# Performance work log

Hardware: AMD Instinct MI355X
Metric: run time of the kernel (lower is better)

Reference implementation:

```python
import jax, jax.numpy as jnp
import numpy as np

HEADS = 4
DIM_HEAD = 32
DIM = 512
HIDDEN = HEADS * DIM_HEAD  # 128


def setup_inputs() -> dict:
    key = jax.random.key(0)
    k1, k2, k3, k4 = jax.random.split(key, 4)
    b, l = 8, 8192
    x = jax.random.normal(k1, (b, DIM, l), dtype=jnp.float32)
    # Conv1d kernel_size=1 weights stored as [out_ch, in_ch] (squeeze kernel dim)
    w_qkv = jax.random.normal(k2, (HIDDEN * 3, DIM), dtype=jnp.float32) * (1.0 / np.sqrt(DIM))
    w_out = jax.random.normal(k3, (DIM, HIDDEN), dtype=jnp.float32) * (1.0 / np.sqrt(HIDDEN))
    b_out = jax.random.normal(k4, (DIM,), dtype=jnp.float32) * 0.01
    return {"x": x, "w_qkv": w_qkv, "w_out": w_out, "b_out": b_out}


def reference(x, w_qkv, w_out, b_out):
    b, c, l = x.shape
    # 1x1 conv == channel matmul: [b, 3*hidden, l]
    qkv = jnp.einsum('oc,bcl->bol', w_qkv, x)
    # split into q, k, v each [b, heads, dim_head, l]
    qkv = qkv.reshape(b, 3, HEADS, DIM_HEAD, l)
    q, k, v = qkv[:, 0], qkv[:, 1], qkv[:, 2]
    k = jax.nn.softmax(k, axis=-1)  # softmax over sequence positions
    # context: [b, h, d, e] (small dim_head x dim_head per head)
    context = jnp.einsum('bhdn,bhen->bhde', k, v)
    out = jnp.einsum('bhde,bhdn->bhen', context, q)  # [b, h, e, l]
    out = out.reshape(b, HIDDEN, l)
    return jnp.einsum('oc,bcl->bol', w_out, out) + b_out[None, :, None]
```

## Files before the change

kernel.cpp:

```cpp
#include <hip/hip_runtime.h>
#include <math.h>
#include <stdint.h>


#define L_LEN 8192L
#define DIMC 512

typedef short bf16x8 __attribute__((ext_vector_type(8)));
typedef float f32x4 __attribute__((ext_vector_type(4)));

__device__ __forceinline__ unsigned short f2bf(float f) {
    uint32_t u = __float_as_uint(f);
    u += 0x7FFFu + ((u >> 16) & 1u);
    return (unsigned short)(u >> 16);
}
__device__ __forceinline__ void unpack8(uint4 u, float* f) {
    f[0] = __uint_as_float(u.x << 16); f[1] = __uint_as_float(u.x & 0xFFFF0000u);
    f[2] = __uint_as_float(u.y << 16); f[3] = __uint_as_float(u.y & 0xFFFF0000u);
    f[4] = __uint_as_float(u.z << 16); f[5] = __uint_as_float(u.z & 0xFFFF0000u);
    f[6] = __uint_as_float(u.w << 16); f[7] = __uint_as_float(u.w & 0xFFFF0000u);
}

#define GLOAD_LDS16(g, l) __builtin_amdgcn_global_load_lds( \
    (const __attribute__((address_space(1))) uint32_t*)(g), \
    (__attribute__((address_space(3))) uint32_t*)(l), 16, 0, 0)

__global__ __launch_bounds__(256)
void misc_kernel(const float* __restrict__ w, unsigned short* __restrict__ wb,
                 float* __restrict__ zbase)
{
    int idx = blockIdx.x * 256 + threadIdx.x;
    if (idx < 196608) wb[idx] = f2bf(w[idx]);
    else {
        int z = idx - 196608;
        if (z < 33792) zbase[z] = 0.0f;
    }
}

__global__ __launch_bounds__(256)
void xpose_cvt_kernel(const float* __restrict__ x, unsigned short* __restrict__ xb)
{
    const int b  = blockIdx.z;
    const int c0 = blockIdx.y * 64;
    const int l0 = blockIdx.x * 64;
    const float* xp = x + (long)b * DIMC * L_LEN;
    unsigned short* op = xb + (long)b * L_LEN * DIMC;
    __shared__ float tile[64][65];
    const int t = threadIdx.x;
    #pragma unroll
    for (int r = 0; r < 4; ++r) {
        int idx = t + 256 * r;
        int row = idx >> 4, col4 = (idx & 15) * 4;
        float4 v = *(const float4*)&xp[(long)(c0 + row) * L_LEN + l0 + col4];
        tile[row][col4 + 0] = v.x;
        tile[row][col4 + 1] = v.y;
        tile[row][col4 + 2] = v.z;
        tile[row][col4 + 3] = v.w;
    }
    __syncthreads();
    #pragma unroll
    for (int r = 0; r < 4; ++r) {
        int idx = t + 256 * r;
        int lr = idx >> 4, c4 = (idx & 15) * 4;
        ushort4 o;
        o.x = f2bf(tile[c4 + 0][lr]);
        o.y = f2bf(tile[c4 + 1][lr]);
        o.z = f2bf(tile[c4 + 2][lr]);
        o.w = f2bf(tile[c4 + 3][lr]);
        *(ushort4*)&op[(long)(l0 + lr) * DIMC + c0 + c4] = o;
    }
}

template<int OUT_BF16, int KD>
__global__ __launch_bounds__(256)
void mfma_gemm_kernel(const unsigned short* __restrict__ A, long aBS,
                      const unsigned short* __restrict__ B, long bBS,
                      void* __restrict__ Cv, long cBS,
                      const float* __restrict__ bias)
{
    const int b  = blockIdx.z;
    const int m0 = blockIdx.y * 128;
    const int l0 = blockIdx.x * 128;
    A += (long)b * aBS;
    B += (long)b * bBS;

    __shared__ unsigned short Asm[2 * 4096];
    __shared__ unsigned short Bsm[2 * 4096];

    const int t = threadIdx.x;
    const int wave = t >> 6, lane = t & 63;
    const int wm = (wave & 1) * 64, wn = (wave >> 1) * 64;
    const int srow  = wave * 16 + (lane >> 2);
    const int skoff = (lane & 3) * 8;
    const int fr = lane & 15, quad = lane >> 4;

    f32x4 acc[4][4] = {};

    for (int k0 = 0; k0 < KD; k0 += 64) {
        #pragma unroll
        for (int c = 0; c < 2; ++c) {
            const int kk = k0 + c * 32 + skoff;
            GLOAD_LDS16(A + (long)(m0 + srow) * KD + kk,      Asm + c * 4096 + wave * 512);
            GLOAD_LDS16(A + (long)(m0 + 64 + srow) * KD + kk, Asm + c * 4096 + 2048 + wave * 512);
            GLOAD_LDS16(B + (long)(l0 + srow) * KD + kk,      Bsm + c * 4096 + wave * 512);
            GLOAD_LDS16(B + (long)(l0 + 64 + srow) * KD + kk, Bsm + c * 4096 + 2048 + wave * 512);
        }
        __syncthreads();

        #pragma unroll
        for (int c = 0; c < 2; ++c) {
            bf16x8 af[4], bf[4];
            #pragma unroll
            for (int i = 0; i < 4; ++i)
                af[i] = *(const bf16x8*)&Asm[c * 4096 + (wm + i * 16 + fr) * 32 + quad * 8];
            #pragma unroll
            for (int j = 0; j < 4; ++j)
                bf[j] = *(const bf16x8*)&Bsm[c * 4096 + (wn + j * 16 + fr) * 32 + quad * 8];
            #pragma unroll
            for (int i = 0; i < 4; ++i)
                #pragma unroll
                for (int j = 0; j < 4; ++j)
                    acc[i][j] = __builtin_amdgcn_mfma_f32_16x16x32_bf16(af[i], bf[j], acc[i][j], 0, 0, 0);
        }
        __syncthreads();
    }

    #pragma unroll
    for (int i = 0; i < 4; ++i) {
        #pragma unroll
        for (int j = 0; j < 4; ++j) {
            #pragma unroll
            for (int r = 0; r < 4; ++r) {
                int m = m0 + wm + i * 16 + quad * 4 + r;
                long l = l0 + wn + j * 16 + fr;
                float v = acc[i][j][r];
                if (bias) v += bias[m];
                if (OUT_BF16)
                    ((unsigned short*)Cv)[(long)b * cBS + (long)m * L_LEN + l] = f2bf(v);
                else
                    ((float*)Cv)[(long)b * cBS + (long)m * L_LEN + l] = v;
            }
        }
    }
}

__global__ __launch_bounds__(256)
void qt_kernel(const unsigned short* __restrict__ qkvb, unsigned short* __restrict__ qT)
{
    const int b   = blockIdx.z;
    const int hd0 = blockIdx.y * 64;
    const int l0  = blockIdx.x * 64;
    const unsigned short* qp = qkvb + (long)b * 384 * L_LEN;
    unsigned short* op = qT + (long)b * L_LEN * 128;
    __shared__ unsigned short tile[64][72];
    const int t = threadIdx.x;
    #pragma unroll
    for (int r = 0; r < 2; ++r) {
        int row = r * 32 + (t >> 3), col8 = (t & 7) * 8;
        uint4 v = *(const uint4*)&qp[(long)(hd0 + row) * L_LEN + l0 + col8];
        *(uint4*)&tile[row][col8] = v;
    }
    __syncthreads();
    const int lr = t >> 2, c16 = (t & 3) * 16;
    unsigned short o[16];
    #pragma unroll
    for (int j = 0; j < 16; ++j) o[j] = tile[c16 + j][lr];
    unsigned short* dst = op + (long)(l0 + lr) * 128 + hd0 + c16;
    *(uint4*)&dst[0] = *(const uint4*)&o[0];
    *(uint4*)&dst[8] = *(const uint4*)&o[8];
}

__global__ __launch_bounds__(256)
void ctx_kernel(const unsigned short* __restrict__ kv, long batchStride, long kOff, long vOff,
                float* __restrict__ ctxU, float* __restrict__ S)
{
    const int bid  = blockIdx.x;
    const int esel = bid & 1;
    const int nc   = (bid >> 1) & 3;
    const int dg   = (bid >> 3) & 7;
    const int h    = (bid >> 6) & 3;
    const int b    = bid >> 8;
    const int d0   = dg * 4, e0 = esel * 16;
    const int t = threadIdx.x;
    const long n = (long)nc * 2048 + t * 8;

    const unsigned short* kp = kv + (long)b * batchStride + kOff + (long)(h * 32 + d0) * L_LEN + n;
    const unsigned short* vp = kv + (long)b * batchStride + vOff + (long)(h * 32 + e0) * L_LEN + n;

    float w8[4][8], s4[4];
    #pragma unroll
    for (int i = 0; i < 4; ++i) {
        uint4 u = *(const uint4*)&kp[(long)i * L_LEN];
        float f[8]; unpack8(u, f);
        float s = 0.0f;
        #pragma unroll
        for (int k = 0; k < 8; ++k) { w8[i][k] = __expf(f[k]); s += w8[i][k]; }
        s4[i] = s;
    }
    float acc[4][16];
    #pragma unroll
    for (int e = 0; e < 16; ++e) {
        uint4 u = *(const uint4*)&vp[(long)e * L_LEN];
        float g[8]; unpack8(u, g);
        #pragma unroll
        for (int i = 0; i < 4; ++i) {
            float s = 0.0f;
            #pragma unroll
            for (int k = 0; k < 8; ++k) s = fmaf(w8[i][k], g[k], s);
            acc[i][e] = s;
        }
    }

    const int wave = t >> 6, lane = t & 63;
    __shared__ float red[4][68];
    #pragma unroll
    for (int i = 0; i < 4; ++i) {
        #pragma unroll
        for (int e = 0; e < 16; ++e) {
            float v = acc[i][e];
            for (int off = 32; off; off >>= 1) v += __shfl_down(v, off, 64);
            if (lane == 0) red[wave][i * 16 + e] = v;
        }
        float sv = s4[i];
        for (int off = 32; off; off >>= 1) sv += __shfl_down(sv, off, 64);
        if (lane == 0) red[wave][64 + i] = sv;
    }
    __syncthreads();
    if (t < 68) {
        float v = red[0][t] + red[1][t] + red[2][t] + red[3][t];
        if (t < 64) {
            int i = t >> 4, e = t & 15;
            atomicAdd(&ctxU[(((long)(b * 4 + h) * 32) + d0 + i) * 32 + e0 + e], v);
        } else if (esel == 0) {
            atomicAdd(&S[b * 128 + h * 32 + d0 + (t - 64)], v);
        }
    }
}

template<int OUT_BF16>
__global__ __launch_bounds__(256)
void w2_kernel(const float* __restrict__ w_out, const float* __restrict__ ctxU,
               const float* __restrict__ S, void* __restrict__ out)
{
    const int idx = blockIdx.x * 256 + threadIdx.x;
    const int b = idx >> 16;
    const int rem = idx & 65535;
    const int o = rem >> 7, hd = rem & 127;
    const int h = hd >> 5, d = hd & 31;
    const float* wp = w_out + o * 128 + h * 32;
    const float* cp = ctxU + (((long)(b * 4 + h) * 32) + d) * 32;
    float s = 0.0f;
    #pragma unroll
    for (int e = 0; e < 32; e += 4) {
        float4 wv = *(const float4*)&wp[e];
        float4 cv = *(const float4*)&cp[e];
        s += wv.x * cv.x + wv.y * cv.y + wv.z * cv.z + wv.w * cv.w;
    }
    s /= S[b * 128 + hd];
    if (OUT_BF16) ((unsigned short*)out)[idx] = f2bf(s);
    else          ((float*)out)[idx] = s;
}

__global__ __launch_bounds__(256)
void weff_kernel(const float* __restrict__ W2, const float* __restrict__ wq,
                 unsigned short* __restrict__ Weffb)
{
    const int b  = blockIdx.z;
    const int ot = blockIdx.y * 64;
    const int ct = blockIdx.x * 64;
    __shared__ float W2t[64][129];
    __shared__ float wqt[128][64];
    const int t = threadIdx.x;
    const float* W2b = W2 + (long)b * 512 * 128;
    #pragma unroll
    for (int r = 0; r < 8; ++r) {
        int f4 = t + 256 * r;
        int row = f4 >> 5, c4 = (f4 & 31) * 4;
        float4 v = *(const float4*)&W2b[(long)(ot + row) * 128 + c4];
        W2t[row][c4 + 0] = v.x; W2t[row][c4 + 1] = v.y;
        W2t[row][c4 + 2] = v.z; W2t[row][c4 + 3] = v.w;
    }
    #pragma unroll
    for (int r = 0; r < 8; ++r) {
        int f4 = t + 256 * r;
        int hd = f4 >> 4, c4 = (f4 & 15) * 4;
        *(float4*)&wqt[hd][c4] = *(const float4*)&wq[(long)hd * DIMC + ct + c4];
    }
    __syncthreads();
    const int oo = (t >> 4) * 4, cc = (t & 15) * 4;
    float acc[4][4] = {};
    for (int hd = 0; hd < 128; ++hd) {
        float a[4], bb[4];
        #pragma unroll
        for (int e = 0; e < 4; ++e) a[e]  = W2t[oo + e][hd];
        #pragma unroll
        for (int e = 0; e < 4; ++e) bb[e] = wqt[hd][cc + e];
        #pragma unroll
        for (int i = 0; i < 4; ++i)
            #pragma unroll
            for (int j = 0; j < 4; ++j)
                acc[i][j] = fmaf(a[i], bb[j], acc[i][j]);
    }
    #pragma unroll
    for (int i = 0; i < 4; ++i)
        #pragma unroll
        for (int j = 0; j < 4; ++j)
            Weffb[((long)b * 512 + ot + oo + i) * 512 + ct + cc + j] = f2bf(acc[i][j]);
}

extern "C" void kernel_launch(void* const* d_in, const int* in_sizes, int n_in,
                              void* d_out, int out_size, void* d_ws, size_t ws_size,
                              hipStream_t stream)
{
    const float* x     = (const float*)d_in[0];
    const float* w_qkv = (const float*)d_in[1];
    const float* w_out = (const float*)d_in[2];
    const float* b_out = (const float*)d_in[3];
    float* out = (float*)d_out;

    char* ws = (char*)d_ws;
    unsigned short* xb = (unsigned short*)ws;

    const bool qpath = (ws_size >= 117968896UL);

    if (qpath) {
        unsigned short* qkvb = (unsigned short*)(ws + 67108864L);
        char* T = ws + 117440512L;
        unsigned short* wb = (unsigned short*)T;
        float* ctxU = (float*)(T + 393216L);
        float* Ssum = (float*)(T + 524288L);
        unsigned short* qT  = xb;
        unsigned short* W2b = qkvb;

        misc_kernel<<<900, 256, 0, stream>>>(w_qkv, wb, ctxU);
        xpose_cvt_kernel<<<dim3(128, 8, 8), 256, 0, stream>>>(x, xb);
        mfma_gemm_kernel<1, 512><<<dim3(64, 3, 8), 256, 0, stream>>>(
            wb, 0L, xb, L_LEN * DIMC, qkvb, 384L * L_LEN, nullptr);
        qt_kernel<<<dim3(128, 2, 8), 256, 0, stream>>>(qkvb, qT);
        ctx_kernel<<<2048, 256, 0, stream>>>(qkvb, 384L * L_LEN, 128L * L_LEN, 256L * L_LEN,
                                             ctxU, Ssum);
        w2_kernel<1><<<2048, 256, 0, stream>>>(w_out, ctxU, Ssum, W2b);
        mfma_gemm_kernel<0, 128><<<dim3(64, 4, 8), 256, 0, stream>>>(
            W2b, 512L * 128, qT, L_LEN * 128, out, 512L * L_LEN, b_out);
    } else {
        unsigned short* kvb = (unsigned short*)(ws + 67108864L);
        char* T = ws + 100663296L;
        unsigned short* wb = (unsigned short*)T;
        float* ctxU = (float*)(T + 393216L);
        float* Ssum = (float*)(T + 524288L);
        unsigned short* Weffb = kvb;
        float* W2f = (float*)(ws + 67108864L + 4194304L);

        misc_kernel<<<900, 256, 0, stream>>>(w_qkv, wb, ctxU);
        xpose_cvt_kernel<<<dim3(128, 8, 8), 256, 0, stream>>>(x, xb);
        mfma_gemm_kernel<1, 512><<<dim3(64, 2, 8), 256, 0, stream>>>(
            wb + 128 * DIMC, 0L, xb, L_LEN * DIMC, kvb, 256L * L_LEN, nullptr);
        ctx_kernel<<<2048, 256, 0, stream>>>(kvb, 256L * L_LEN, 0L, 128L * L_LEN,
                                             ctxU, Ssum);
        w2_kernel<0><<<2048, 256, 0, stream>>>(w_out, ctxU, Ssum, W2f);
        weff_kernel<<<dim3(8, 8, 8), 256, 0, stream>>>(W2f, w_qkv, Weffb);
        mfma_gemm_kernel<0, 512><<<dim3(64, 4, 8), 256, 0, stream>>>(
            Weffb, 512L * DIMC, xb, L_LEN * DIMC, out, 512L * L_LEN, b_out);
    }
}
```

Measured before the change: 385.7 us.

## Fuse Q transpose into QKV GEMM epilogue and vectorize GEMM stores

The QKV GEMM now writes the Q rows (m0==0 blocks) directly in transposed [l,128] layout through an LDS staging tile, so the separate qt_kernel launch and its extra read/write pass go away. The MFMA operand order is swapped, which leaves each lane holding four consecutive l-positions for one output row. The general epilogue uses that to emit ushort4/float4 vector stores with the bias hoisted per row. Workspace aliasing changes: W2b moves to xb and the final GEMM reads qT from the qkvb buffer, which adds aliasing risk.

```diff
diff --git a/kernel.cpp b/kernel.cpp
--- a/kernel.cpp
+++ b/kernel.cpp
@@ -71,7 +71,7 @@
     }
 }
 
-template<int OUT_BF16, int KD>
+template<int OUT_BF16, int KD, int FUSE_QT>
 __global__ __launch_bounds__(256)
 void mfma_gemm_kernel(const unsigned short* __restrict__ A, long aBS,
                       const unsigned short* __restrict__ B, long bBS,
@@ -84,8 +84,9 @@
     A += (long)b * aBS;
     B += (long)b * bBS;
 
-    __shared__ unsigned short Asm[2 * 4096];
-    __shared__ unsigned short Bsm[2 * 4096];
+    __shared__ unsigned short SMEM[16384];
+    unsigned short* Asm = SMEM;
+    unsigned short* Bsm = SMEM + 8192;
 
     const int t = threadIdx.x;
     const int wave = t >> 6, lane = t & 63;
@@ -120,54 +121,48 @@
             for (int i = 0; i < 4; ++i)
                 #pragma unroll
                 for (int j = 0; j < 4; ++j)
-                    acc[i][j] = __builtin_amdgcn_mfma_f32_16x16x32_bf16(af[i], bf[j], acc[i][j], 0, 0, 0);
+                    acc[i][j] = __builtin_amdgcn_mfma_f32_16x16x32_bf16(bf[j], af[i], acc[i][j], 0, 0, 0);
         }
         __syncthreads();
     }
 
-    #pragma unroll
-    for (int i = 0; i < 4; ++i) {
-        #pragma unroll
-        for (int j = 0; j < 4; ++j) {
-            #pragma unroll
-            for (int r = 0; r < 4; ++r) {
-                int m = m0 + wm + i * 16 + quad * 4 + r;
-                long l = l0 + wn + j * 16 + fr;
-                float v = acc[i][j][r];
-                if (bias) v += bias[m];
-                if (OUT_BF16)
-                    ((unsigned short*)Cv)[(long)b * cBS + (long)m * L_LEN + l] = f2bf(v);
-                else
-                    ((float*)Cv)[(long)b * cBS + (long)m * L_LEN + l] = v;
+    if (FUSE_QT && m0 == 0) {
+        #pragma unroll
+        for (int i = 0; i < 4; ++i)
+            #pragma unroll
+            for (int j = 0; j < 4; ++j)
+                #pragma unroll
+                for (int r = 0; r < 4; ++r)
+                    SMEM[(wn + j * 16 + quad * 4 + r) * 128 + wm + i * 16 + fr] =
+                        f2bf(acc[i][j][r]);
+        __syncthreads();
+        unsigned short* qT = (unsigned short*)Cv + (long)b * cBS;
+        #pragma unroll
+        for (int rep = 0; rep < 8; ++rep) {
+            int idx = rep * 256 + t;
+            int row = idx >> 4, c8 = (idx & 15) * 8;
+            *(uint4*)&qT[(long)(l0 + row) * 128 + c8] = *(const uint4*)&SMEM[row * 128 + c8];
+        }
+    } else {
+        #pragma unroll
+        for (int i = 0; i < 4; ++i) {
+            const int m = m0 + wm + i * 16 + fr;
+            const float bv = bias ? bias[m] : 0.0f;
+            #pragma unroll
+            for (int j = 0; j < 4; ++j) {
+                const long lbase = l0 + wn + j * 16 + quad * 4;
+                float v0 = acc[i][j][0] + bv, v1 = acc[i][j][1] + bv;
+                float v2 = acc[i][j][2] + bv, v3 = acc[i][j][3] + bv;
+                if (OUT_BF16) {
+                    ushort4 o; o.x = f2bf(v0); o.y = f2bf(v1); o.z = f2bf(v2); o.w = f2bf(v3);
+                    *(ushort4*)&((unsigned short*)Cv)[(long)b * cBS + (long)m * L_LEN + lbase] = o;
+                } else {
+                    float4 o; o.x = v0; o.y = v1; o.z = v2; o.w = v3;
+                    *(float4*)&((float*)Cv)[(long)b * cBS + (long)m * L_LEN + lbase] = o;
+                }
             }
         }
     }
-}
-
-__global__ __launch_bounds__(256)
-void qt_kernel(const unsigned short* __restrict__ qkvb, unsigned short* __restrict__ qT)
-{
-    const int b   = blockIdx.z;
-    const int hd0 = blockIdx.y * 64;
-    const int l0  = blockIdx.x * 64;
-    const unsigned short* qp = qkvb + (long)b * 384 * L_LEN;
-    unsigned short* op = qT + (long)b * L_LEN * 128;
-    __shared__ unsigned short tile[64][72];
-    const int t = threadIdx.x;
-    #pragma unroll
-    for (int r = 0; r < 2; ++r) {
-        int row = r * 32 + (t >> 3), col8 = (t & 7) * 8;
-        uint4 v = *(const uint4*)&qp[(long)(hd0 + row) * L_LEN + l0 + col8];
-        *(uint4*)&tile[row][col8] = v;
-    }
-    __syncthreads();
-    const int lr = t >> 2, c16 = (t & 3) * 16;
-    unsigned short o[16];
-    #pragma unroll
-    for (int j = 0; j < 16; ++j) o[j] = tile[c16 + j][lr];
-    unsigned short* dst = op + (long)(l0 + lr) * 128 + hd0 + c16;
-    *(uint4*)&dst[0] = *(const uint4*)&o[0];
-    *(uint4*)&dst[8] = *(const uint4*)&o[8];
 }
 
 __global__ __launch_bounds__(256)
@@ -329,19 +324,17 @@
         unsigned short* wb = (unsigned short*)T;
         float* ctxU = (float*)(T + 393216L);
         float* Ssum = (float*)(T + 524288L);
-        unsigned short* qT  = xb;
-        unsigned short* W2b = qkvb;
+        unsigned short* W2b = xb;
 
         misc_kernel<<<900, 256, 0, stream>>>(w_qkv, wb, ctxU);
         xpose_cvt_kernel<<<dim3(128, 8, 8), 256, 0, stream>>>(x, xb);
-        mfma_gemm_kernel<1, 512><<<dim3(64, 3, 8), 256, 0, stream>>>(
+        mfma_gemm_kernel<1, 512, 1><<<dim3(64, 3, 8), 256, 0, stream>>>(
             wb, 0L, xb, L_LEN * DIMC, qkvb, 384L * L_LEN, nullptr);
-        qt_kernel<<<dim3(128, 2, 8), 256, 0, stream>>>(qkvb, qT);
         ctx_kernel<<<2048, 256, 0, stream>>>(qkvb, 384L * L_LEN, 128L * L_LEN, 256L * L_LEN,
                                              ctxU, Ssum);
         w2_kernel<1><<<2048, 256, 0, stream>>>(w_out, ctxU, Ssum, W2b);
-        mfma_gemm_kernel<0, 128><<<dim3(64, 4, 8), 256, 0, stream>>>(
-            W2b, 512L * 128, qT, L_LEN * 128, out, 512L * L_LEN, b_out);
+        mfma_gemm_kernel<0, 128, 0><<<dim3(64, 4, 8), 256, 0, stream>>>(
+            W2b, 512L * 128, qkvb, 384L * L_LEN, out, 512L * L_LEN, b_out);
     } else {
         unsigned short* kvb = (unsigned short*)(ws + 67108864L);
         char* T = ws + 100663296L;
@@ -353,13 +346,13 @@
 
         misc_kernel<<<900, 256, 0, stream>>>(w_qkv, wb, ctxU);
         xpose_cvt_kernel<<<dim3(128, 8, 8), 256, 0, stream>>>(x, xb);
-        mfma_gemm_kernel<1, 512><<<dim3(64, 2, 8), 256, 0, stream>>>(
+        mfma_gemm_kernel<1, 512, 0><<<dim3(64, 2, 8), 256, 0, stream>>>(
             wb + 128 * DIMC, 0L, xb, L_LEN * DIMC, kvb, 256L * L_LEN, nullptr);
         ctx_kernel<<<2048, 256, 0, stream>>>(kvb, 256L * L_LEN, 0L, 128L * L_LEN,
                                              ctxU, Ssum);
         w2_kernel<0><<<2048, 256, 0, stream>>>(w_out, ctxU, Ssum, W2f);
         weff_kernel<<<dim3(8, 8, 8), 256, 0, stream>>>(W2f, w_qkv, Weffb);
-        mfma_gemm_kernel<0, 512><<<dim3(64, 4, 8), 256, 0, stream>>>(
+        mfma_gemm_kernel<0, 512, 0><<<dim3(64, 4, 8), 256, 0, stream>>>(
             Weffb, 512L * DIMC, xb, L_LEN * DIMC, out, 512L * L_LEN, b_out);
     }
 }
```

Result: faster. 362.1 us (-6.1%).
